# Performance work log

Hardware: AMD Instinct MI355X
Metric: run time of the kernel (lower is better)

Reference implementation:

```python
import jax, jax.numpy as jnp
import numpy as np

B, S, HID = 4, 4096, 2048
H = 16            # num_attention_heads
P = 256           # page_size
D = HID // H      # head_dim = 128
N = S // P        # num pages = 16
SCALE = D ** -0.5


def setup_inputs() -> dict:
    key = jax.random.key(0)
    ks = jax.random.split(key, 9)
    w = lambda k: (jax.random.normal(k, (HID, HID), jnp.float32) * 0.02)
    return {
        "hidden_states": jax.random.normal(ks[0], (B, S, HID), jnp.float32),
        "Wq": w(ks[1]), "bq": jnp.zeros((HID,), jnp.float32),
        "Wk": w(ks[2]), "bk": jnp.zeros((HID,), jnp.float32),
        "Wv": w(ks[3]), "bv": jnp.zeros((HID,), jnp.float32),
        "Wo": w(ks[4]), "bo": jnp.zeros((HID,), jnp.float32),
    }


def _heads(y):
    # (B,S,HID) -> (B,H,S,D)  [mirrors _reshape]
    return jnp.transpose(y.reshape(B, S, H, D), (0, 2, 1, 3))


def _paged(x):
    # torch: x.unfold(2, P, P) -> (B,H,N,D,P); then .reshape(-1,H,P,D)
    # reinterprets the row-major flat buffer. Reproduce exactly.
    u = jnp.swapaxes(x.reshape(B, H, N, P, D), -1, -2)  # (B,H,N,D,P)
    return u.reshape(B * N, H, P, D)


def reference(hidden_states, Wq, bq, Wk, bk, Wv, bv, Wo, bo):
    q = _heads(hidden_states @ Wq.T + bq)
    k = _heads(hidden_states @ Wk.T + bk)
    v = _heads(hidden_states @ Wv.T + bv)
    q, k, v = _paged(q), _paged(k), _paged(v)  # (B*N, H, P, D) each

    scores = jnp.einsum("xhqd,xhkd->xhqk", q, k) * SCALE  # (B*N,H,P,P)
    probs = jax.nn.softmax(scores, axis=-1)
    ctx = jnp.einsum("xhqk,xhkd->xhqd", probs, v)         # (B*N,H,P,D)

    # ctx.transpose(1,2).view(b, -1, hidden)
    ctx = jnp.transpose(ctx, (0, 2, 1, 3)).reshape(B, N * P, HID)
    return ctx @ Wo.T + bo
```

## Files before the change

### kernel.cpp

```cpp
#include <hip/hip_runtime.h>


typedef unsigned short u16;
typedef unsigned int u32;
typedef __attribute__((ext_vector_type(8))) __bf16 bf16x8;
typedef __attribute__((ext_vector_type(4))) float f32x4;
typedef __attribute__((ext_vector_type(8))) u16 u16x8;

struct alignas(8) U4 { u16 x, y, z, w; };

#define SCALE_ 0.08838834764831845f

__device__ __forceinline__ u16 f2bf(float f) {
  union { float f; u32 u; } v; v.f = f;
  u32 r = v.u + 0x7fffu + ((v.u >> 16) & 1u);
  return (u16)(r >> 16);
}

__device__ __forceinline__ void glds16(const void* g, void* l) {
  __builtin_amdgcn_global_load_lds(
      (const __attribute__((address_space(1))) u32*)g,
      (__attribute__((address_space(3))) u32*)l, 16, 0, 0);
}

__global__ void cvt_kernel(const float* __restrict__ src, u16* __restrict__ dst, int n4) {
  int i = blockIdx.x * 256 + threadIdx.x;
  if (i >= n4) return;
  float4 f = ((const float4*)src)[i];
  U4 o = { f2bf(f.x), f2bf(f.y), f2bf(f.z), f2bf(f.w) };
  ((U4*)dst)[i] = o;
}


#define MFMA_Q(AF, BF, MB, NB) do { \
  _Pragma("unroll") for (int mt_ = 0; mt_ < 4; ++mt_) \
  _Pragma("unroll") for (int nt_ = 0; nt_ < 2; ++nt_) \
  _Pragma("unroll") for (int kh_ = 0; kh_ < 2; ++kh_) \
    acc[(MB)+mt_][(NB)+nt_] = __builtin_amdgcn_mfma_f32_16x16x32_bf16( \
      AF[mt_][kh_], BF[nt_][kh_], acc[(MB)+mt_][(NB)+nt_], 0, 0, 0); \
} while (0)

#define LDA(F, MTB, BUF) do { \
  _Pragma("unroll") for (int mt_ = 0; mt_ < 4; ++mt_) { \
    F[mt_][0] = *(const bf16x8*)(aRd0 + (BUF)*65536 + ((MTB)+mt_)*2048); \
    F[mt_][1] = *(const bf16x8*)(aRd1 + (BUF)*65536 + ((MTB)+mt_)*2048); \
  } } while (0)

#define LDB(F, NTB, BUF) do { \
  _Pragma("unroll") for (int nt_ = 0; nt_ < 2; ++nt_) { \
    F[nt_][0] = *(const bf16x8*)(bRd0 + (BUF)*65536 + ((NTB)+nt_)*2048); \
    F[nt_][1] = *(const bf16x8*)(bRd1 + (BUF)*65536 + ((NTB)+nt_)*2048); \
  } } while (0)

#define STAGE_A(BUF, H, KK) do { \
  glds16(Asrc + (size_t)((H)*128) * 2048 + (KK), dstA + (BUF)*65536 + (H)*16384); \
  glds16(Asrc + (size_t)((H)*128 + 64) * 2048 + (KK), dstA + (BUF)*65536 + (H)*16384 + 8192); \
} while (0)

#define STAGE_B(BUF, H, KK) do { \
  glds16(Bsrc + (size_t)((H)*128) * 2048 + (KK), dstB + (BUF)*65536 + (H)*16384); \
  glds16(Bsrc + (size_t)((H)*128 + 64) * 2048 + (KK), dstB + (BUF)*65536 + (H)*16384 + 8192); \
} while (0)

#define PH_ENTER() do { \
  __builtin_amdgcn_s_barrier(); \
  asm volatile("s_waitcnt lgkmcnt(0)" ::: "memory"); \
  __builtin_amdgcn_sched_barrier(0); \
  __builtin_amdgcn_s_setprio(1); \
} while (0)

#define PH_EXIT() do { \
  __builtin_amdgcn_s_setprio(0); \
  __builtin_amdgcn_sched_barrier(0); \
  __builtin_amdgcn_s_barrier(); \
} while (0)

#define PH_EXIT_VM(N) do { \
  __builtin_amdgcn_s_setprio(0); \
  __builtin_amdgcn_sched_barrier(0); \
  asm volatile("s_waitcnt vmcnt(" #N ")" ::: "memory"); \
  __builtin_amdgcn_s_barrier(); \
} while (0)

#define LGKM_HINT() asm volatile("s_waitcnt lgkmcnt(8)" ::: "memory")

__global__ __launch_bounds__(512, 2) void gemm_kernel(
    const u16* __restrict__ A, const u16* __restrict__ Bw,
    const float* __restrict__ bias, void* __restrict__ outp, int mode)
{
  extern __shared__ char Sm[];
  const int tid  = threadIdx.x;
  const int lane = tid & 63;
  const int wid  = tid >> 6;
  const int L    = lane & 15;
  const int quad = lane >> 4;
  const int wm   = wid >> 2;
  const int wn   = wid & 3;
  const int m0 = (int)(blockIdx.x >> 3) << 8;
  const int n0 = (int)(blockIdx.x & 7) << 8;

  const int srow = tid >> 3;
  const int scs  = (tid & 7) ^ (srow & 7);
  const u16* Asrc = A  + (size_t)(m0 + srow) * 2048 + scs * 8;
  const u16* Bsrc = Bw + (size_t)(n0 + srow) * 2048 + scs * 8;
  char* dstA = Sm + tid * 16;
  char* dstB = Sm + 32768 + tid * 16;

  const int xA = ((quad ^ (L & 7)) << 4);
  const char* aRd0 = Sm + (wm * 128 + L) * 128 + xA;
  const char* aRd1 = Sm + (wm * 128 + L) * 128 + (xA ^ 64);
  const char* bRd0 = Sm + 32768 + (wn * 64 + L) * 128 + xA;
  const char* bRd1 = Sm + 32768 + (wn * 64 + L) * 128 + (xA ^ 64);

  f32x4 acc[8][4];
#pragma unroll
  for (int i = 0; i < 8; ++i)
#pragma unroll
    for (int j = 0; j < 4; ++j)
      acc[i][j] = f32x4{0.f, 0.f, 0.f, 0.f};

  bf16x8 aLo[4][2], aHi[4][2], bLo[2][2], bHi[2][2];

  STAGE_A(0, 0, 0);
  STAGE_A(0, 1, 0);
  STAGE_B(0, 0, 0);
  STAGE_B(0, 1, 0);
  STAGE_A(1, 0, 64);
  STAGE_A(1, 1, 64);
  asm volatile("s_waitcnt vmcnt(4)" ::: "memory");
  __builtin_amdgcn_s_barrier();

#pragma unroll 1
  for (int it = 0; it < 16; ++it) {
    const int kb = it * 128;
    LDA(aLo, 0, 0); LDB(bLo, 0, 0);
    STAGE_B(1, 0, kb + 64);
    LGKM_HINT();
    PH_ENTER();
    MFMA_Q(aLo, bLo, 0, 0);
    PH_EXIT();
    LDA(aHi, 4, 0); LDB(bHi, 2, 0);
    STAGE_B(1, 1, kb + 64);
    LGKM_HINT();
    PH_ENTER();
    MFMA_Q(aLo, bHi, 0, 2);
    PH_EXIT();
    if (it < 15) STAGE_A(0, 0, kb + 128);
    PH_ENTER();
    MFMA_Q(aHi, bLo, 4, 0);
    PH_EXIT();
    if (it < 15) STAGE_A(0, 1, kb + 128);
    PH_ENTER();
    MFMA_Q(aHi, bHi, 4, 2);
    if (it < 15) { PH_EXIT_VM(4); } else { PH_EXIT_VM(0); }
    LDA(aLo, 0, 1); LDB(bLo, 0, 1);
    if (it < 15) STAGE_B(0, 0, kb + 128);
    LGKM_HINT();
    PH_ENTER();
    MFMA_Q(aLo, bLo, 0, 0);
    PH_EXIT();
    LDA(aHi, 4, 1); LDB(bHi, 2, 1);
    if (it < 15) STAGE_B(0, 1, kb + 128);
    LGKM_HINT();
    PH_ENTER();
    MFMA_Q(aLo, bHi, 0, 2);
    PH_EXIT();
    if (it < 15) STAGE_A(1, 0, kb + 192);
    PH_ENTER();
    MFMA_Q(aHi, bLo, 4, 0);
    PH_EXIT();
    if (it < 15) STAGE_A(1, 1, kb + 192);
    PH_ENTER();
    MFMA_Q(aHi, bHi, 4, 2);
    PH_EXIT_VM(4);
  }

#pragma unroll
  for (int nt = 0; nt < 4; ++nt) {
    const int c = n0 + wn * 64 + nt * 16 + L;
    const float bv = bias[c];
    const int h = c >> 7, d = c & 127;
#pragma unroll
    for (int mt = 0; mt < 8; ++mt) {
      const int sg = m0 + wm * 128 + mt * 16 + (quad << 2);
      const int b   = sg >> 12;
      const int s   = sg & 4095;
      const int npg = (s >> 8) & 15;
      const int half = (s >> 7) & 1;
      const int plo  = s & 127;
      const f32x4 v = acc[mt][nt];
      const size_t bb = ((size_t)((b * 16 + h) * 16 + npg)) << 15;
      if (mode == 0) {
        U4 o = { f2bf(v[0] + bv), f2bf(v[1] + bv), f2bf(v[2] + bv), f2bf(v[3] + bv) };
        *(U4*)((u16*)outp + bb + (size_t)(2 * d + half) * 128 + plo) = o;
      } else if (mode == 1) {
        u16* o16 = (u16*)outp + bb + 2 * d + half;
        o16[(size_t)(plo + 0) * 256] = f2bf(v[0] + bv);
        o16[(size_t)(plo + 1) * 256] = f2bf(v[1] + bv);
        o16[(size_t)(plo + 2) * 256] = f2bf(v[2] + bv);
        o16[(size_t)(plo + 3) * 256] = f2bf(v[3] + bv);
      } else {
        float* of = (float*)outp + (size_t)sg * 2048 + c;
        of[0]    = v[0] + bv;
        of[2048] = v[1] + bv;
        of[4096] = v[2] + bv;
        of[6144] = v[3] + bv;
      }
    }
  }
}

__global__ __launch_bounds__(1024, 4) void attn_kernel(
    const u16* __restrict__ Qp, const u16* __restrict__ Kp,
    const u16* __restrict__ Vt, u16* __restrict__ ctx)
{
  __shared__ u16 Sm[32768];
  const int tid  = threadIdx.x;
  const int wid  = tid >> 6;
  const int lane = tid & 63;
  const int L    = lane & 15;
  const int quad = lane >> 4;
  const int pg   = blockIdx.x;
  const int x2 = pg >> 4, h2 = pg & 15;
  const int q0 = wid * 16;

  const char* Qb = (const char*)(Qp + (size_t)pg * 32768);
  const char* Kb = (const char*)(Kp + (size_t)pg * 32768);
  const char* Vb = (const char*)(Vt + (size_t)pg * 32768);

#pragma unroll
  for (int r = 0; r < 4; ++r) {
    const int u = tid + (r << 10);
    const int row = u >> 4, cc = u & 15;
    glds16(Kb + (size_t)(row * 16 + (cc ^ (row & 15))) * 16, (char*)Sm + u * 16);
  }

  bf16x8 qf[4];
#pragma unroll
  for (int kt = 0; kt < 4; ++kt)
    qf[kt] = *(const bf16x8*)(Qb + (q0 + L) * 256 + kt * 64 + quad * 16);

  __syncthreads();

  f32x4 st[16];
#pragma unroll
  for (int mt = 0; mt < 16; ++mt) st[mt] = f32x4{0.f, 0.f, 0.f, 0.f};
#pragma unroll
  for (int kt = 0; kt < 4; ++kt) {
    const int c = kt * 4 + quad;
#pragma unroll
    for (int mt = 0; mt < 16; ++mt) {
      bf16x8 a = *(const bf16x8*)((const char*)Sm + (mt * 16 + L) * 256 + ((c ^ L) << 4));
      st[mt] = __builtin_amdgcn_mfma_f32_16x16x32_bf16(a, qf[kt], st[mt], 0, 0, 0);
    }
  }

  float mx = -3.0e38f;
#pragma unroll
  for (int mt = 0; mt < 16; ++mt) {
    mx = fmaxf(mx, st[mt][0]); mx = fmaxf(mx, st[mt][1]);
    mx = fmaxf(mx, st[mt][2]); mx = fmaxf(mx, st[mt][3]);
  }
  mx = fmaxf(mx, __shfl_xor(mx, 16));
  mx = fmaxf(mx, __shfl_xor(mx, 32));
  float sum = 0.f;
#pragma unroll
  for (int mt = 0; mt < 16; ++mt) {
#pragma unroll
    for (int r = 0; r < 4; ++r) {
      float e = __expf((st[mt][r] - mx) * SCALE_);
      st[mt][r] = e;
      sum += e;
    }
  }
  sum += __shfl_xor(sum, 16);
  sum += __shfl_xor(sum, 32);
  const float rinv = 1.f / sum;

  __syncthreads();
#pragma unroll
  for (int r = 0; r < 4; ++r) {
    const int u = tid + (r << 10);
    const int row = u >> 5, cc = u & 31;
    glds16(Vb + (size_t)(row * 32 + (cc ^ (row & 15))) * 16, (char*)Sm + u * 16);
  }
  __syncthreads();

  f32x4 ct[8];
#pragma unroll
  for (int mt = 0; mt < 8; ++mt) ct[mt] = f32x4{0.f, 0.f, 0.f, 0.f};
#pragma unroll
  for (int kt = 0; kt < 8; ++kt) {
    u16x8 pt;
#pragma unroll
    for (int j = 0; j < 8; ++j) {
      const int src = ((quad & 1) * 2 + (j >> 2)) * 16 + L;
      float v0 = __shfl(st[2 * kt][j & 3], src);
      float v1 = __shfl(st[2 * kt + 1][j & 3], src);
      pt[j] = f2bf(quad < 2 ? v0 : v1);
    }
    bf16x8 pb = __builtin_bit_cast(bf16x8, pt);
    const int c = kt * 4 + quad;
#pragma unroll
    for (int mt = 0; mt < 8; ++mt) {
      bf16x8 a = *(const bf16x8*)((const char*)Sm + (mt * 16 + L) * 512 + ((c ^ L) << 4));
      ct[mt] = __builtin_amdgcn_mfma_f32_16x16x32_bf16(a, pb, ct[mt], 0, 0, 0);
    }
  }

  const int b = x2 >> 4, h = x2 & 15;
  const int sg = h * 256 + q0 + L;
  u16* orow = ctx + ((size_t)b * 4096 + sg) * 2048 + h2 * 128;
#pragma unroll
  for (int mt = 0; mt < 8; ++mt) {
    U4 o = { f2bf(ct[mt][0] * rinv), f2bf(ct[mt][1] * rinv),
             f2bf(ct[mt][2] * rinv), f2bf(ct[mt][3] * rinv) };
    *(U4*)(orow + mt * 16 + quad * 4) = o;
  }
}

extern "C" void kernel_launch(void* const* d_in, const int* in_sizes, int n_in,
                              void* d_out, int out_size, void* d_ws, size_t ws_size,
                              hipStream_t stream) {
  const float* X  = (const float*)d_in[0];
  const float* Wq = (const float*)d_in[1];
  const float* bq = (const float*)d_in[2];
  const float* Wk = (const float*)d_in[3];
  const float* bk = (const float*)d_in[4];
  const float* Wv = (const float*)d_in[5];
  const float* bv = (const float*)d_in[6];
  const float* Wo = (const float*)d_in[7];
  const float* bo = (const float*)d_in[8];

  static bool attr_set = false;
  if (!attr_set) {
    hipFuncSetAttribute((const void*)gemm_kernel,
                        hipFuncAttributeMaxDynamicSharedMemorySize, 131072);
    attr_set = true;
  }

  char* ws = (char*)d_ws;
  u16* Xb  = (u16*)(ws);
  u16* Wqb = (u16*)(ws + 67108864);
  u16* Wkb = (u16*)(ws + 75497472);
  u16* Wvb = (u16*)(ws + 83886080);
  u16* Wob = (u16*)(ws + 92274688);
  u16* Qp  = (u16*)(ws + 100663296);
  u16* Kp  = (u16*)(ws + 167772160);
  u16* Vt  = (u16*)(ws + 234881024);
  u16* Cb  = (u16*)(ws + 301989888);

  cvt_kernel<<<32768, 256, 0, stream>>>(X,  Xb,  8388608);
  cvt_kernel<<<4096,  256, 0, stream>>>(Wq, Wqb, 1048576);
  cvt_kernel<<<4096,  256, 0, stream>>>(Wk, Wkb, 1048576);
  cvt_kernel<<<4096,  256, 0, stream>>>(Wv, Wvb, 1048576);
  cvt_kernel<<<4096,  256, 0, stream>>>(Wo, Wob, 1048576);

  gemm_kernel<<<512, 512, 131072, stream>>>(Xb, Wqb, bq, (void*)Qp, 0);
  gemm_kernel<<<512, 512, 131072, stream>>>(Xb, Wkb, bk, (void*)Kp, 0);
  gemm_kernel<<<512, 512, 131072, stream>>>(Xb, Wvb, bv, (void*)Vt, 1);

  attn_kernel<<<1024, 1024, 0, stream>>>(Qp, Kp, Vt, Cb);

  gemm_kernel<<<512, 512, 131072, stream>>>(Cb, Wob, bo, d_out, 2);
}
```

Measured before the change: 897.9 us.

## Batch QKV GEMMs into one launch, remap tiles per XCD, deepen prefetch

The three Q/K/V projection GEMMs become one launch with a second grid dimension that selects weight, bias, output and mode. The four weight conversions are merged into one launch. Block-to-tile mapping is changed so each XCD handles a contiguous group of M tiles, aiming for better L2 reuse of A rows. The K-loop staging is restructured so both B halves are prefetched one stage earlier, with vmcnt waits raised to match; this adds more loads in flight and risks pipeline hazards.

```diff
diff --git a/kernel.cpp b/kernel.cpp
--- a/kernel.cpp
+++ b/kernel.cpp
@@ -31,6 +31,19 @@
   ((U4*)dst)[i] = o;
 }
 
+__global__ void cvtw_kernel(const float* __restrict__ s0, const float* __restrict__ s1,
+                            const float* __restrict__ s2, const float* __restrict__ s3,
+                            u16* __restrict__ d0, int n4) {
+  const int w = blockIdx.y;
+  const float* src = (w == 0) ? s0 : (w == 1) ? s1 : (w == 2) ? s2 : s3;
+  u16* dst = d0 + (size_t)w * 4194304;
+  int i = blockIdx.x * 256 + threadIdx.x;
+  if (i >= n4) return;
+  float4 f = ((const float4*)src)[i];
+  U4 o = { f2bf(f.x), f2bf(f.y), f2bf(f.z), f2bf(f.w) };
+  ((U4*)dst)[i] = o;
+}
+
 
 #define MFMA_Q(AF, BF, MB, NB) do { \
   _Pragma("unroll") for (int mt_ = 0; mt_ < 4; ++mt_) \
@@ -85,10 +98,19 @@
 #define LGKM_HINT() asm volatile("s_waitcnt lgkmcnt(8)" ::: "memory")
 
 __global__ __launch_bounds__(512, 2) void gemm_kernel(
-    const u16* __restrict__ A, const u16* __restrict__ Bw,
-    const float* __restrict__ bias, void* __restrict__ outp, int mode)
+    const u16* __restrict__ A,
+    const u16* __restrict__ W0, const u16* __restrict__ W1, const u16* __restrict__ W2,
+    const float* __restrict__ b0, const float* __restrict__ b1, const float* __restrict__ b2,
+    void* __restrict__ o0, void* __restrict__ o1, void* __restrict__ o2,
+    int md0, int md1, int md2)
 {
   extern __shared__ char Sm[];
+  const int g = blockIdx.y;
+  const u16* Bw     = (g == 0) ? W0 : (g == 1) ? W1 : W2;
+  const float* bias = (g == 0) ? b0 : (g == 1) ? b1 : b2;
+  void* outp        = (g == 0) ? o0 : (g == 1) ? o1 : o2;
+  const int mode    = (g == 0) ? md0 : (g == 1) ? md1 : md2;
+
   const int tid  = threadIdx.x;
   const int lane = tid & 63;
   const int wid  = tid >> 6;
@@ -96,8 +118,11 @@
   const int quad = lane >> 4;
   const int wm   = wid >> 2;
   const int wn   = wid & 3;
-  const int m0 = (int)(blockIdx.x >> 3) << 8;
-  const int n0 = (int)(blockIdx.x & 7) << 8;
+  const int bid = blockIdx.x;
+  const int xcd = bid & 7;
+  const int idx = bid >> 3;
+  const int m0 = (xcd * 8 + (idx & 7)) << 8;
+  const int n0 = (idx >> 3) << 8;
 
   const int srow = tid >> 3;
   const int scs  = (tid & 7) ^ (srow & 7);
@@ -127,52 +152,50 @@
   STAGE_B(0, 1, 0);
   STAGE_A(1, 0, 64);
   STAGE_A(1, 1, 64);
-  asm volatile("s_waitcnt vmcnt(4)" ::: "memory");
+  STAGE_B(1, 0, 64);
+  STAGE_B(1, 1, 64);
+  asm volatile("s_waitcnt vmcnt(8)" ::: "memory");
   __builtin_amdgcn_s_barrier();
 
 #pragma unroll 1
   for (int it = 0; it < 16; ++it) {
     const int kb = it * 128;
     LDA(aLo, 0, 0); LDB(bLo, 0, 0);
-    STAGE_B(1, 0, kb + 64);
     LGKM_HINT();
     PH_ENTER();
     MFMA_Q(aLo, bLo, 0, 0);
     PH_EXIT();
     LDA(aHi, 4, 0); LDB(bHi, 2, 0);
-    STAGE_B(1, 1, kb + 64);
     LGKM_HINT();
     PH_ENTER();
     MFMA_Q(aLo, bHi, 0, 2);
     PH_EXIT();
-    if (it < 15) STAGE_A(0, 0, kb + 128);
+    if (it < 15) { STAGE_A(0, 0, kb + 128); STAGE_A(0, 1, kb + 128); }
     PH_ENTER();
     MFMA_Q(aHi, bLo, 4, 0);
     PH_EXIT();
-    if (it < 15) STAGE_A(0, 1, kb + 128);
+    if (it < 15) { STAGE_B(0, 0, kb + 128); STAGE_B(0, 1, kb + 128); }
     PH_ENTER();
     MFMA_Q(aHi, bHi, 4, 2);
-    if (it < 15) { PH_EXIT_VM(4); } else { PH_EXIT_VM(0); }
+    if (it < 15) { PH_EXIT_VM(8); } else { PH_EXIT_VM(0); }
     LDA(aLo, 0, 1); LDB(bLo, 0, 1);
-    if (it < 15) STAGE_B(0, 0, kb + 128);
     LGKM_HINT();
     PH_ENTER();
     MFMA_Q(aLo, bLo, 0, 0);
     PH_EXIT();
     LDA(aHi, 4, 1); LDB(bHi, 2, 1);
-    if (it < 15) STAGE_B(0, 1, kb + 128);
     LGKM_HINT();
     PH_ENTER();
     MFMA_Q(aLo, bHi, 0, 2);
     PH_EXIT();
-    if (it < 15) STAGE_A(1, 0, kb + 192);
+    if (it < 15) { STAGE_A(1, 0, kb + 192); STAGE_A(1, 1, kb + 192); }
     PH_ENTER();
     MFMA_Q(aHi, bLo, 4, 0);
     PH_EXIT();
-    if (it < 15) STAGE_A(1, 1, kb + 192);
+    if (it < 15) { STAGE_B(1, 0, kb + 192); STAGE_B(1, 1, kb + 192); }
     PH_ENTER();
     MFMA_Q(aHi, bHi, 4, 2);
-    PH_EXIT_VM(4);
+    if (it < 15) { PH_EXIT_VM(8); } else { PH_EXIT(); }
   }
 
 #pragma unroll
@@ -342,25 +365,22 @@
   char* ws = (char*)d_ws;
   u16* Xb  = (u16*)(ws);
   u16* Wqb = (u16*)(ws + 67108864);
-  u16* Wkb = (u16*)(ws + 75497472);
-  u16* Wvb = (u16*)(ws + 83886080);
-  u16* Wob = (u16*)(ws + 92274688);
   u16* Qp  = (u16*)(ws + 100663296);
   u16* Kp  = (u16*)(ws + 167772160);
   u16* Vt  = (u16*)(ws + 234881024);
   u16* Cb  = (u16*)(ws + 301989888);
-
-  cvt_kernel<<<32768, 256, 0, stream>>>(X,  Xb,  8388608);
-  cvt_kernel<<<4096,  256, 0, stream>>>(Wq, Wqb, 1048576);
-  cvt_kernel<<<4096,  256, 0, stream>>>(Wk, Wkb, 1048576);
-  cvt_kernel<<<4096,  256, 0, stream>>>(Wv, Wvb, 1048576);
-  cvt_kernel<<<4096,  256, 0, stream>>>(Wo, Wob, 1048576);
-
-  gemm_kernel<<<512, 512, 131072, stream>>>(Xb, Wqb, bq, (void*)Qp, 0);
-  gemm_kernel<<<512, 512, 131072, stream>>>(Xb, Wkb, bk, (void*)Kp, 0);
-  gemm_kernel<<<512, 512, 131072, stream>>>(Xb, Wvb, bv, (void*)Vt, 1);
+  u16* Wkb = Wqb + 4194304;
+  u16* Wvb = Wqb + 8388608;
+  u16* Wob = Wqb + 12582912;
+
+  cvt_kernel<<<32768, 256, 0, stream>>>(X, Xb, 8388608);
+  cvtw_kernel<<<dim3(4096, 4), 256, 0, stream>>>(Wq, Wk, Wv, Wo, Wqb, 1048576);
+
+  gemm_kernel<<<dim3(512, 3), 512, 131072, stream>>>(
+      Xb, Wqb, Wkb, Wvb, bq, bk, bv, (void*)Qp, (void*)Kp, (void*)Vt, 0, 0, 1);
 
   attn_kernel<<<1024, 1024, 0, stream>>>(Qp, Kp, Vt, Cb);
 
-  gemm_kernel<<<512, 512, 131072, stream>>>(Cb, Wob, bo, d_out, 2);
-}
+  gemm_kernel<<<dim3(512, 1), 512, 131072, stream>>>(
+      Cb, Wob, Wob, Wob, bo, bo, bo, d_out, d_out, d_out, 2, 2, 2);
+}
```

After: 890.8 us. No clear change (-0.8%).
